# Optimization experiments

Hardware: AMD Instinct MI355X
Metric: run time of the kernel (lower is better)

The kernel has to match this reference:

```python
import jax, jax.numpy as jnp
import numpy as np

B, N, L, G, H, D, DIM = 32, 512, 4096, 128, 8, 1, 64
ALPHA = 3.0


def setup_inputs() -> dict:
    key = jax.random.key(0)
    k = jax.random.split(key, 8)
    return {
        "idx": jnp.arange(N, dtype=jnp.int32),
        "queries": jnp.zeros((1,), jnp.float32),
        "keys": jnp.zeros((1,), jnp.float32),
        "values": jnp.zeros((1,), jnp.float32),
        "attn_mask": jnp.zeros((1,), jnp.bool_),
        "x": jax.random.normal(k[0], (B, N, L), jnp.float32),
        "emb1": jax.random.normal(k[1], (N, DIM), jnp.float32),
        "emb2": jax.random.normal(k[2], (N, DIM), jnp.float32),
        "lin1_w": jax.random.normal(k[3], (DIM, DIM), jnp.float32) / np.sqrt(DIM).astype(np.float32),
        "lin1_b": jnp.zeros((DIM,), jnp.float32),
        "lin2_w": jax.random.normal(k[4], (DIM, DIM), jnp.float32) / np.sqrt(DIM).astype(np.float32),
        "lin2_b": jnp.zeros((DIM,), jnp.float32),
        "mlp_w": jax.random.normal(k[5], (L, H * D), jnp.float32) / np.sqrt(L).astype(np.float32),
        "mlp_b": jnp.zeros((H * D,), jnp.float32),
        "W_sel": jax.random.normal(k[6], (H, G, D), jnp.float32),
    }


def reference(idx, queries, keys, values, attn_mask, x,
              emb1, emb2, lin1_w, lin1_b, lin2_w, lin2_b,
              mlp_w, mlp_b, W_sel):
    # --- graph_constructor.forward(idx) ---
    n1 = jnp.tanh(ALPHA * (emb1[idx] @ lin1_w + lin1_b))   # [N, DIM]
    n2 = jnp.tanh(ALPHA * (emb2[idx] @ lin2_w + lin2_b))   # [N, DIM]
    a = n1 @ n2.T - n2 @ n1.T                               # [N, N]
    adj = jnp.tanh(ALPHA * a)
    # topk (k == nsensor in GlobalAttention) + scatter mask; noise in the
    # original only perturbs tie-breaking of indices, values are set to 1.
    kk = idx.shape[0]
    _, top_idx = jax.lax.top_k(adj, kk)
    rows = jnp.arange(adj.shape[0])[:, None]
    mask = jnp.zeros_like(adj).at[rows, top_idx].set(1.0)
    adj = adj * mask

    # --- SelectAttention(x) ---
    b, n, l = x.shape
    newx = jnp.tanh(x.reshape(b * n, l) @ mlp_w + mlp_b)    # [(B N), H*D]
    # faithful raw row-major reshape (matches torch.reshape semantics)
    newx = newx.reshape(b, H, n, D)                          # [B, H, N, D]
    sel = jax.nn.relu(jnp.einsum('bhnd,hgd->bhng', newx, W_sel))[:, 0]  # [B, N, G]

    # --- combine ---
    scores = jnp.einsum('ls,blg->bsg', adj, sel)             # [B, N, G]
    series = jax.nn.softmax(scores, axis=-1)
    V = jnp.einsum('bls,blg->bsg', x, series)                # [B, L, G]
    return V
```

## Files before the change

kernel.cpp:

```cpp
#include <hip/hip_runtime.h>
#include <hip/hip_bf16.h>
#include <math.h>

#define BB 32
#define NN 512
#define LL 4096
#define GG 128
#define DD 64
#define RS 20
#define AS 36

typedef __attribute__((ext_vector_type(4))) float f32x4;
typedef __attribute__((ext_vector_type(8))) short bf16x8;
typedef __attribute__((ext_vector_type(4))) unsigned u32x4;
typedef __attribute__((ext_vector_type(4))) unsigned short u16x4;

__device__ inline float sx(float v, int m) { return __shfl_xor(v, m, 64); }

__global__ __launch_bounds__(64) void ga_nodes(
    const int* __restrict__ idx,
    const float* __restrict__ emb1, const float* __restrict__ emb2,
    const float* __restrict__ w1, const float* __restrict__ b1,
    const float* __restrict__ w2, const float* __restrict__ b2,
    float* __restrict__ n1, float* __restrict__ n2) {
  int i = blockIdx.x;
  int d = threadIdx.x;
  int ii = idx[i];
  const float* e1 = emb1 + ii * DD;
  const float* e2 = emb2 + ii * DD;
  float a1 = 0.f, a2 = 0.f;
  #pragma unroll 8
  for (int k = 0; k < DD; ++k) {
    a1 += e1[k] * w1[k * DD + d];
    a2 += e2[k] * w2[k * DD + d];
  }
  n1[i * DD + d] = tanhf(3.f * (a1 + b1[d]));
  n2[i * DD + d] = tanhf(3.f * (a2 + b2[d]));
}

__global__ __launch_bounds__(256) void ga_adjT(
    const float* __restrict__ n1, const float* __restrict__ n2,
    __hip_bfloat16* __restrict__ adjT16) {
  int r = blockIdx.x;
  __shared__ float n1r[DD], n2r[DD];
  if (threadIdx.x < DD) {
    n1r[threadIdx.x] = n1[r * DD + threadIdx.x];
    n2r[threadIdx.x] = n2[r * DD + threadIdx.x];
  }
  __syncthreads();
  for (int l = threadIdx.x; l < NN; l += 256) {
    const float4* p1 = (const float4*)(n1 + l * DD);
    const float4* p2 = (const float4*)(n2 + l * DD);
    float d1 = 0.f, d2 = 0.f;
    #pragma unroll
    for (int q = 0; q < DD / 4; ++q) {
      float4 v1 = p1[q], v2 = p2[q];
      float4 m2 = ((const float4*)n2r)[q];
      float4 m1 = ((const float4*)n1r)[q];
      d1 += v1.x * m2.x + v1.y * m2.y + v1.z * m2.z + v1.w * m2.w;
      d2 += v2.x * m1.x + v2.y * m1.y + v2.z * m1.z + v2.w * m1.w;
    }
    adjT16[r * NN + l] = __float2bfloat16(tanhf(3.f * (d1 - d2)));
  }
}

__global__ __launch_bounds__(256) void ga_mlp(
    const float* __restrict__ x, const float* __restrict__ mlp_w,
    const float* __restrict__ mlp_b, const float* __restrict__ wsel,
    __hip_bfloat16* __restrict__ RT) {
  int b = blockIdx.y;
  int j0 = blockIdx.x * 8;
  int n0 = j0 * 8;
  int tid = threadIdx.x;
  float acc[8][8];
  #pragma unroll
  for (int j = 0; j < 8; ++j)
    #pragma unroll
    for (int c = 0; c < 8; ++c) acc[j][c] = 0.f;

  const float* xb = x + (size_t)b * NN * LL;
  for (int lc = 0; lc < LL; lc += 256) {
    int l = lc + tid;
    float4 w0 = *(const float4*)(mlp_w + l * 8);
    float4 w1 = *(const float4*)(mlp_w + l * 8 + 4);
    #pragma unroll
    for (int j = 0; j < 8; ++j) {
      float xv = xb[(size_t)(j0 + j) * LL + l];
      acc[j][0] += xv * w0.x; acc[j][1] += xv * w0.y;
      acc[j][2] += xv * w0.z; acc[j][3] += xv * w0.w;
      acc[j][4] += xv * w1.x; acc[j][5] += xv * w1.y;
      acc[j][6] += xv * w1.z; acc[j][7] += xv * w1.w;
    }
  }
  #pragma unroll
  for (int j = 0; j < 8; ++j)
    #pragma unroll
    for (int c = 0; c < 8; ++c) {
      float v = acc[j][c];
      for (int off = 32; off; off >>= 1) v += __shfl_down(v, off);
      acc[j][c] = v;
    }
  __shared__ float red[4 * 64];
  __shared__ float tl[64];
  int lane = tid & 63, wave = tid >> 6;
  if (lane == 0) {
    #pragma unroll
    for (int j = 0; j < 8; ++j)
      #pragma unroll
      for (int c = 0; c < 8; ++c) red[wave * 64 + j * 8 + c] = acc[j][c];
  }
  __syncthreads();
  if (tid < 64) {
    float s = red[tid] + red[64 + tid] + red[128 + tid] + red[192 + tid];
    tl[tid] = tanhf(s + mlp_b[tid & 7]);
  }
  __syncthreads();
  unsigned short* rp = (unsigned short*)RT + (size_t)b * GG * NN + n0;
  #pragma unroll
  for (int it = 0; it < 8; ++it) {
    int f = it * 256 + tid;
    int g = f >> 4, c = f & 15;
    float w = wsel[g];
    u16x4 pk;
    #pragma unroll
    for (int k = 0; k < 4; ++k)
      pk[k] = __bfloat16_as_ushort(__float2bfloat16(fmaxf(tl[4 * c + k] * w, 0.f)));
    *(u16x4*)(rp + (size_t)g * NN + 4 * c) = pk;
  }
}

__global__ __launch_bounds__(256) void ga_scores_mfma(
    const __hip_bfloat16* __restrict__ adjT16,
    const __hip_bfloat16* __restrict__ RT,
    __hip_bfloat16* __restrict__ seriesT) {
  int b = blockIdx.y;
  int s0 = blockIdx.x * 128;
  int tid = threadIdx.x;
  __shared__ unsigned As[128 * AS];
  __shared__ unsigned Bs[128 * AS];
  int wave = tid >> 6, lane = tid & 63, q = lane >> 4, mrow = lane & 15;
  const unsigned short* ap = (const unsigned short*)adjT16;
  const unsigned short* bp = (const unsigned short*)RT + (size_t)b * GG * NN;

  f32x4 acc[2][8];
  #pragma unroll
  for (int mf = 0; mf < 2; ++mf)
    #pragma unroll
    for (int nf = 0; nf < 8; ++nf) acc[mf][nf] = (f32x4){0.f, 0.f, 0.f, 0.f};

  for (int l0 = 0; l0 < NN; l0 += 64) {
    #pragma unroll
    for (int it = 0; it < 4; ++it) {
      int ci = it * 256 + tid;
      int row = ci >> 3, part = ci & 7;
      u32x4 va = *(const u32x4*)(ap + (size_t)(s0 + row) * NN + l0 + part * 8);
      u32x4 vb = *(const u32x4*)(bp + (size_t)row * NN + l0 + part * 8);
      *(u32x4*)&As[row * AS + part * 4] = va;
      *(u32x4*)&Bs[row * AS + part * 4] = vb;
    }
    __syncthreads();
    #pragma unroll
    for (int ks = 0; ks < 2; ++ks) {
      bf16x8 af0 = *(const bf16x8*)&As[(wave * 32 + mrow) * AS + ks * 16 + q * 4];
      bf16x8 af1 = *(const bf16x8*)&As[(wave * 32 + 16 + mrow) * AS + ks * 16 + q * 4];
      #pragma unroll
      for (int nf = 0; nf < 8; ++nf) {
        bf16x8 bfr = *(const bf16x8*)&Bs[(nf * 16 + mrow) * AS + ks * 16 + q * 4];
        acc[0][nf] = __builtin_amdgcn_mfma_f32_16x16x32_bf16(af0, bfr, acc[0][nf], 0, 0, 0);
        acc[1][nf] = __builtin_amdgcn_mfma_f32_16x16x32_bf16(af1, bfr, acc[1][nf], 0, 0, 0);
      }
    }
    __syncthreads();
  }

  unsigned short* sT = (unsigned short*)seriesT + (size_t)b * GG * NN;
  #pragma unroll
  for (int mf = 0; mf < 2; ++mf) {
    f32x4 mx = acc[mf][0];
    #pragma unroll
    for (int nf = 1; nf < 8; ++nf)
      #pragma unroll
      for (int r = 0; r < 4; ++r) mx[r] = fmaxf(mx[r], acc[mf][nf][r]);
    #pragma unroll
    for (int m = 1; m <= 8; m <<= 1)
      #pragma unroll
      for (int r = 0; r < 4; ++r) mx[r] = fmaxf(mx[r], sx(mx[r], m));
    f32x4 sum = (f32x4){0.f, 0.f, 0.f, 0.f};
    #pragma unroll
    for (int nf = 0; nf < 8; ++nf)
      #pragma unroll
      for (int r = 0; r < 4; ++r) {
        float e = __expf(acc[mf][nf][r] - mx[r]);
        acc[mf][nf][r] = e;
        sum[r] += e;
      }
    #pragma unroll
    for (int m = 1; m <= 8; m <<= 1)
      #pragma unroll
      for (int r = 0; r < 4; ++r) sum[r] += sx(sum[r], m);
    f32x4 inv;
    #pragma unroll
    for (int r = 0; r < 4; ++r) inv[r] = 1.f / sum[r];
    int sbase = s0 + wave * 32 + mf * 16 + q * 4;
    #pragma unroll
    for (int nf = 0; nf < 8; ++nf) {
      u16x4 pk;
      #pragma unroll
      for (int r = 0; r < 4; ++r)
        pk[r] = __bfloat16_as_ushort(__float2bfloat16(acc[mf][nf][r] * inv[r]));
      *(u16x4*)(sT + (size_t)(nf * 16 + mrow) * NN + sbase) = pk;
    }
  }
}

__global__ __launch_bounds__(256) void ga_V_mfma(
    const float* __restrict__ x, const __hip_bfloat16* __restrict__ seriesT,
    float* __restrict__ out) {
  int b = blockIdx.y;
  int p0 = blockIdx.x * 128;
  int tid = threadIdx.x;

  __shared__ unsigned Xt[128 * RS];
  __shared__ unsigned St[128 * RS];

  int i = tid & 31;
  int j = tid >> 5;
  int wave = tid >> 6, lane = tid & 63, q = lane >> 4, mrow = lane & 15;

  const float* xb = x + (size_t)b * NN * LL + p0;
  const unsigned short* sb = (const unsigned short*)seriesT + (size_t)b * GG * NN;

  f32x4 acc[2][8];
  #pragma unroll
  for (int mf = 0; mf < 2; ++mf)
    #pragma unroll
    for (int nf = 0; nf < 8; ++nf) acc[mf][nf] = (f32x4){0.f, 0.f, 0.f, 0.f};

  for (int l0 = 0; l0 < NN; l0 += 32) {
    #pragma unroll
    for (int h = 0; h < 2; ++h) {
      int lp = j + 8 * h;
      const float* xr0 = xb + (size_t)(l0 + 2 * lp) * LL;
      const float* xr1 = xr0 + LL;
      #pragma unroll
      for (int c = 0; c < 4; ++c) {
        int p = i + 32 * c;
        __hip_bfloat162 pk = __float22bfloat162_rn(make_float2(xr0[p], xr1[p]));
        Xt[p * RS + lp] = *(unsigned*)&pk;
      }
    }
    {
      int c0 = tid;
      int g = c0 >> 2, part = c0 & 3;
      *(u32x4*)&St[g * RS + part * 4] =
          *(const u32x4*)(sb + (size_t)g * NN + l0 + part * 8);
      int c1 = tid + 256;
      g = c1 >> 2; part = c1 & 3;
      *(u32x4*)&St[g * RS + part * 4] =
          *(const u32x4*)(sb + (size_t)g * NN + l0 + part * 8);
    }
    __syncthreads();

    bf16x8 af[2];
    #pragma unroll
    for (int mf = 0; mf < 2; ++mf) {
      int row = wave * 32 + mf * 16 + mrow;
      af[mf] = *(const bf16x8*)&Xt[row * RS + q * 4];
    }
    #pragma unroll
    for (int nf = 0; nf < 8; ++nf) {
      bf16x8 bfr = *(const bf16x8*)&St[(nf * 16 + mrow) * RS + q * 4];
      acc[0][nf] = __builtin_amdgcn_mfma_f32_16x16x32_bf16(af[0], bfr, acc[0][nf], 0, 0, 0);
      acc[1][nf] = __builtin_amdgcn_mfma_f32_16x16x32_bf16(af[1], bfr, acc[1][nf], 0, 0, 0);
    }
    __syncthreads();
  }

  #pragma unroll
  for (int mf = 0; mf < 2; ++mf) {
    int pb = p0 + wave * 32 + mf * 16 + q * 4;
    #pragma unroll
    for (int nf = 0; nf < 8; ++nf) {
      int g = nf * 16 + mrow;
      float* op = out + ((size_t)b * LL + pb) * GG + g;
      #pragma unroll
      for (int r = 0; r < 4; ++r) op[(size_t)r * GG] = acc[mf][nf][r];
    }
  }
}

extern "C" void kernel_launch(void* const* d_in, const int* in_sizes, int n_in,
                              void* d_out, int out_size, void* d_ws, size_t ws_size,
                              hipStream_t stream) {
  const int*   idx    = (const int*)d_in[0];
  const float* x      = (const float*)d_in[5];
  const float* emb1   = (const float*)d_in[6];
  const float* emb2   = (const float*)d_in[7];
  const float* lin1_w = (const float*)d_in[8];
  const float* lin1_b = (const float*)d_in[9];
  const float* lin2_w = (const float*)d_in[10];
  const float* lin2_b = (const float*)d_in[11];
  const float* mlp_w  = (const float*)d_in[12];
  const float* mlp_b  = (const float*)d_in[13];
  const float* W_sel  = (const float*)d_in[14];
  float* out = (float*)d_out;

  float* ws = (float*)d_ws;
  float* n1 = ws;
  float* n2 = ws + 32768;
  __hip_bfloat16* adjT16  = (__hip_bfloat16*)(ws + 65536);
  __hip_bfloat16* RT      = (__hip_bfloat16*)(ws + 196608);
  __hip_bfloat16* seriesT = (__hip_bfloat16*)(ws + 1245184);

  ga_nodes<<<NN, 64, 0, stream>>>(idx, emb1, emb2, lin1_w, lin1_b,
                                  lin2_w, lin2_b, n1, n2);
  ga_adjT<<<NN, 256, 0, stream>>>(n1, n2, adjT16);
  ga_mlp<<<dim3(8, BB), 256, 0, stream>>>(x, mlp_w, mlp_b, W_sel, RT);
  ga_scores_mfma<<<dim3(4, BB), 256, 0, stream>>>(adjT16, RT, seriesT);
  ga_V_mfma<<<dim3(LL / 128, BB), 256, 0, stream>>>(x, seriesT, out);
}
```

Baseline: 127.0 us.

## Double-buffer LDS tiles and prefetch next x/series tile into registers

Restructures the ga_V_mfma main loop into a software pipeline. Global loads for the next 32-row tile of x and seriesT go into registers while the current tile's MFMAs run, and two LDS buffers alternate. The aim is to overlap the global-memory latency of the large x stream with tensor-core work, instead of load → sync → compute → sync on every tile. The cost is more registers for the prefetch buffers and double the LDS footprint, which may lower occupancy.

```diff
diff --git a/kernel.cpp b/kernel.cpp
--- a/kernel.cpp
+++ b/kernel.cpp
@@ -220,12 +220,14 @@
   int p0 = blockIdx.x * 128;
   int tid = threadIdx.x;
 
-  __shared__ unsigned Xt[128 * RS];
-  __shared__ unsigned St[128 * RS];
+  __shared__ unsigned Xt[2][128 * RS];
+  __shared__ unsigned St[2][128 * RS];
 
   int i = tid & 31;
   int j = tid >> 5;
   int wave = tid >> 6, lane = tid & 63, q = lane >> 4, mrow = lane & 15;
+  int sg0 = tid >> 2, spart = tid & 3;
+  int sg1 = sg0 + 64;
 
   const float* xb = x + (size_t)b * NN * LL + p0;
   const unsigned short* sb = (const unsigned short*)seriesT + (size_t)b * GG * NN;
@@ -236,7 +238,10 @@
     #pragma unroll
     for (int nf = 0; nf < 8; ++nf) acc[mf][nf] = (f32x4){0.f, 0.f, 0.f, 0.f};
 
-  for (int l0 = 0; l0 < NN; l0 += 32) {
+  float xvA[2][4][2], xvB[2][4][2];
+  u32x4 svA[2], svB[2];
+
+  auto PRELOAD = [&](float (&xv)[2][4][2], u32x4 (&sv)[2], int l0) {
     #pragma unroll
     for (int h = 0; h < 2; ++h) {
       int lp = j + 8 * h;
@@ -245,35 +250,54 @@
       #pragma unroll
       for (int c = 0; c < 4; ++c) {
         int p = i + 32 * c;
-        __hip_bfloat162 pk = __float22bfloat162_rn(make_float2(xr0[p], xr1[p]));
-        Xt[p * RS + lp] = *(unsigned*)&pk;
+        xv[h][c][0] = xr0[p];
+        xv[h][c][1] = xr1[p];
       }
     }
-    {
-      int c0 = tid;
-      int g = c0 >> 2, part = c0 & 3;
-      *(u32x4*)&St[g * RS + part * 4] =
-          *(const u32x4*)(sb + (size_t)g * NN + l0 + part * 8);
-      int c1 = tid + 256;
-      g = c1 >> 2; part = c1 & 3;
-      *(u32x4*)&St[g * RS + part * 4] =
-          *(const u32x4*)(sb + (size_t)g * NN + l0 + part * 8);
-    }
-    __syncthreads();
-
+    sv[0] = *(const u32x4*)(sb + (size_t)sg0 * NN + l0 + spart * 8);
+    sv[1] = *(const u32x4*)(sb + (size_t)sg1 * NN + l0 + spart * 8);
+  };
+
+  auto WRITE = [&](const float (&xv)[2][4][2], const u32x4 (&sv)[2],
+                   unsigned* XtB, unsigned* StB) {
+    #pragma unroll
+    for (int h = 0; h < 2; ++h) {
+      int lp = j + 8 * h;
+      #pragma unroll
+      for (int c = 0; c < 4; ++c) {
+        int p = i + 32 * c;
+        __hip_bfloat162 pk = __float22bfloat162_rn(make_float2(xv[h][c][0], xv[h][c][1]));
+        XtB[p * RS + lp] = *(unsigned*)&pk;
+      }
+    }
+    *(u32x4*)&StB[sg0 * RS + spart * 4] = sv[0];
+    *(u32x4*)&StB[sg1 * RS + spart * 4] = sv[1];
+  };
+
+  auto COMPUTE = [&](const unsigned* XtB, const unsigned* StB) {
     bf16x8 af[2];
     #pragma unroll
-    for (int mf = 0; mf < 2; ++mf) {
-      int row = wave * 32 + mf * 16 + mrow;
-      af[mf] = *(const bf16x8*)&Xt[row * RS + q * 4];
-    }
+    for (int mf = 0; mf < 2; ++mf)
+      af[mf] = *(const bf16x8*)&XtB[(wave * 32 + mf * 16 + mrow) * RS + q * 4];
     #pragma unroll
     for (int nf = 0; nf < 8; ++nf) {
-      bf16x8 bfr = *(const bf16x8*)&St[(nf * 16 + mrow) * RS + q * 4];
+      bf16x8 bfr = *(const bf16x8*)&StB[(nf * 16 + mrow) * RS + q * 4];
       acc[0][nf] = __builtin_amdgcn_mfma_f32_16x16x32_bf16(af[0], bfr, acc[0][nf], 0, 0, 0);
       acc[1][nf] = __builtin_amdgcn_mfma_f32_16x16x32_bf16(af[1], bfr, acc[1][nf], 0, 0, 0);
     }
+  };
+
+  PRELOAD(xvA, svA, 0);
+  #pragma unroll 1
+  for (int tt = 0; tt < 8; ++tt) {
+    WRITE(xvA, svA, Xt[0], St[0]);
+    if (tt < 8) PRELOAD(xvB, svB, (2 * tt + 1) * 32);
     __syncthreads();
+    COMPUTE(Xt[0], St[0]);
+    WRITE(xvB, svB, Xt[1], St[1]);
+    if (tt < 7) PRELOAD(xvA, svA, (2 * tt + 2) * 32);
+    __syncthreads();
+    COMPUTE(Xt[1], St[1]);
   }
 
   #pragma unroll
```

After: 129.4 us. About the same (+1.9%).
